# Performance work log

Hardware: AMD Instinct MI355X
Metric: run time of the kernel (lower is better)

Reference implementation:

```python
import jax, jax.numpy as jnp
import numpy as np

D_MODEL = 1024
N_HEADS = 16
D_HEAD = D_MODEL // N_HEADS
SCALE = D_HEAD ** 0.5
EPS_NORM = 1e-10
EPS_CLAMP = 1e-06


def _sphere(x):
    # project to unit sphere along last dim
    n = jnp.maximum(jnp.linalg.norm(x, axis=-1, keepdims=True), EPS_NORM)
    return x / n


def setup_inputs() -> dict:
    key = jax.random.key(0)
    ks = jax.random.split(key, 9)
    s = 1.0 / np.sqrt(D_MODEL)  # torch Linear default init scale
    inp = {
        "H": jax.random.normal(ks[0], (2, 2048, D_MODEL), dtype=jnp.float32),
        "W_q": jax.random.uniform(ks[1], (D_MODEL, D_MODEL), jnp.float32, -s, s),
        "b_q": jax.random.uniform(ks[2], (D_MODEL,), jnp.float32, -s, s),
        "W_k": jax.random.uniform(ks[3], (D_MODEL, D_MODEL), jnp.float32, -s, s),
        "b_k": jax.random.uniform(ks[4], (D_MODEL,), jnp.float32, -s, s),
        "W_v": jax.random.uniform(ks[5], (D_MODEL, D_MODEL), jnp.float32, -s, s),
        "b_v": jax.random.uniform(ks[6], (D_MODEL,), jnp.float32, -s, s),
        "W_o": jax.random.uniform(ks[7], (D_MODEL, D_MODEL), jnp.float32, -s, s),
        "b_o": jax.random.uniform(ks[8], (D_MODEL,), jnp.float32, -s, s),
    }
    return inp


def reference(H, W_q, b_q, W_k, b_k, W_v, b_v, W_o, b_o):
    B, S, _ = H.shape
    # torch Linear: y = x @ W.T + b
    def proj(W, b):
        y = jnp.einsum('bsd,ed->bse', H, W) + b
        return _sphere(y.reshape(B, S, N_HEADS, D_HEAD).transpose(0, 2, 1, 3))  # [B,H,S,Dh]
    Q = proj(W_q, b_q)
    K = proj(W_k, b_k)
    V = proj(W_v, b_v)
    cos = jnp.einsum('bhqd,bhkd->bhqk', Q, K)
    cos = jnp.clip(cos, -1.0 + EPS_CLAMP, 1.0 - EPS_CLAMP)
    scores = -jnp.arccos(cos) / SCALE
    attn = jax.nn.softmax(scores, axis=-1)
    out = jnp.einsum('bhqk,bhkd->bhqd', attn, V)
    out = out.transpose(0, 2, 1, 3).reshape(B, S, D_MODEL)
    return jnp.einsum('bsd,ed->bse', out, W_o) + b_o
```

## Files before the change

### kernel.cpp

```cpp
#include <hip/hip_runtime.h>
#include <hip/hip_bf16.h>

typedef __bf16 bf16_t;
typedef __bf16 bf16x8 __attribute__((ext_vector_type(8)));
typedef __bf16 bf16x4 __attribute__((ext_vector_type(4)));
typedef float f32x2 __attribute__((ext_vector_type(2)));
typedef float f32x4 __attribute__((ext_vector_type(4)));
typedef float f32x16 __attribute__((ext_vector_type(16)));

#define NB 2
#define SEQ 2048
#define DMODEL 1024
#define NHEAD 16
#define DHEAD 64

#define PSWAP(x, y) asm("v_permlane32_swap_b32 %0, %1" : "+v"(x), "+v"(y))
#define CVTPK(d, a, b) asm("v_cvt_pk_bf16_f32 %0, %1, %2" : "=v"(d) : "v"(a), "v"(b))
#define WAITVM(n) asm volatile("s_waitcnt vmcnt(" #n ")" ::: "memory")

__device__ inline void gload_lds16(const void* g, void* lds) {
  __builtin_amdgcn_global_load_lds((const __attribute__((address_space(1))) void*)g,
                                   (__attribute__((address_space(3))) void*)lds,
                                   16, 0, 0);
}

__global__ __launch_bounds__(256) void cvt_all_kernel(
    const float* __restrict__ H,  const float* __restrict__ Wq, const float* __restrict__ Wk,
    const float* __restrict__ Wv, const float* __restrict__ Wo,
    bf16_t* __restrict__ Hb, bf16_t* __restrict__ Wqb, bf16_t* __restrict__ Wkb,
    bf16_t* __restrict__ Wvb, bf16_t* __restrict__ Wob)
{
  const int b = blockIdx.x;
  const float* src; bf16_t* dst; int idx;
  if (b < 4096) { src = H; dst = Hb; idx = b; }
  else {
    const int r = b - 4096; const int s = r >> 10; idx = r & 1023;
    src = (s == 0) ? Wq : (s == 1) ? Wk : (s == 2) ? Wv : Wo;
    dst = (s == 0) ? Wqb : (s == 1) ? Wkb : (s == 2) ? Wvb : Wob;
  }
  const int i = idx * 256 + threadIdx.x;
  float4 v = ((const float4*)src)[i];
  bf16x4 o;
  o[0] = (bf16_t)v.x; o[1] = (bf16_t)v.y; o[2] = (bf16_t)v.z; o[3] = (bf16_t)v.w;
  ((bf16x4*)dst)[i] = o;
}

template<int MODE>
__global__ __launch_bounds__(256, 3) void gemm_bt_kernel(
    const bf16_t* __restrict__ A,
    const bf16_t* __restrict__ W0, const bf16_t* __restrict__ W1, const bf16_t* __restrict__ W2,
    const float* __restrict__ bias0, const float* __restrict__ bias1, const float* __restrict__ bias2,
    void* out0, void* out1, void* out2)
{
  __shared__ char gsm[49152];
  const int tid = threadIdx.x;
  const int lane = tid & 63;
  const int w = tid >> 6;
  const int mt = blockIdx.y, nt = blockIdx.x, z = blockIdx.z;
  const bf16_t* Wp = (z == 0) ? W0 : ((z == 1) ? W1 : W2);
  const float* bp  = (z == 0) ? bias0 : ((z == 1) ? bias1 : bias2);

  const int wr = w & 1, wc = w >> 1;
  const int fr = lane & 15, fq = lane >> 4;

  const int r_in = lane >> 3;
  const int cswz = ((lane & 7) ^ (r_in & 7)) << 4;

  f32x4 acc[2][4] = {};

  const char* Ab = (const char*)(A + (size_t)mt * 64 * DMODEL);
  const char* Bb = (const char*)(Wp + (size_t)nt * 128 * DMODEL);

  const unsigned aA0 = (unsigned)__builtin_amdgcn_readfirstlane(w * 2048);
  const unsigned bB0 = (unsigned)__builtin_amdgcn_readfirstlane(16384 + w * 4096);

  #define GSTAGE(t, buf)                                                                   \
    do {                                                                                   \
      const size_t k0b_ = (size_t)(t) * 128;                                               \
      _Pragma("unroll")                                                                    \
      for (int i = 0; i < 2; ++i) {                                                        \
        const size_t rowA_ = (size_t)(w * 16 + i * 8 + r_in);                              \
        gload_lds16(Ab + rowA_ * (DMODEL * 2) + k0b_ + cswz,                               \
                    gsm + aA0 + (buf) * 8192 + i * 1024);                                  \
      }                                                                                    \
      _Pragma("unroll")                                                                    \
      for (int i = 0; i < 4; ++i) {                                                        \
        const size_t rowB_ = (size_t)(w * 32 + i * 8 + r_in);                              \
        gload_lds16(Bb + rowB_ * (DMODEL * 2) + k0b_ + cswz,                               \
                    gsm + bB0 + (buf) * 16384 + i * 1024);                                 \
      }                                                                                    \
    } while (0)

  #define GCOMPUTE(buf)                                                                    \
    do {                                                                                   \
      const char* As_ = gsm + (buf) * 8192;                                                \
      const char* Bs_ = gsm + 16384 + (buf) * 16384;                                       \
      bf16x8 a_[2][2], b_[4][2];                                                           \
      _Pragma("unroll")                                                                    \
      for (int m = 0; m < 2; ++m)                                                          \
        _Pragma("unroll")                                                                  \
        for (int ks = 0; ks < 2; ++ks)                                                     \
          a_[m][ks] = *(const bf16x8*)(As_ + (wr * 32 + m * 16 + fr) * 128 +               \
                                       ((ks * 64 + fq * 16) ^ ((fr & 7) << 4)));           \
      _Pragma("unroll")                                                                    \
      for (int n = 0; n < 4; ++n)                                                          \
        _Pragma("unroll")                                                                  \
        for (int ks = 0; ks < 2; ++ks)                                                     \
          b_[n][ks] = *(const bf16x8*)(Bs_ + (wc * 64 + n * 16 + fr) * 128 +               \
                                       ((ks * 64 + fq * 16) ^ ((fr & 7) << 4)));           \
      __builtin_amdgcn_s_setprio(1);                                                       \
      _Pragma("unroll")                                                                    \
      for (int m = 0; m < 2; ++m)                                                          \
        _Pragma("unroll")                                                                  \
        for (int n = 0; n < 4; ++n)                                                        \
          _Pragma("unroll")                                                                \
          for (int ks = 0; ks < 2; ++ks)                                                   \
            acc[m][n] = __builtin_amdgcn_mfma_f32_16x16x32_bf16(a_[m][ks], b_[n][ks],      \
                                                                acc[m][n], 0, 0, 0);       \
      __builtin_amdgcn_s_setprio(0);                                                       \
    } while (0)

  GSTAGE(0, 0);
  GSTAGE(1, 1);
  for (int t2 = 0; t2 < 7; ++t2) {
    WAITVM(6);
    __builtin_amdgcn_s_barrier();
    GCOMPUTE(0);
    __builtin_amdgcn_s_barrier();
    GSTAGE(2 * t2 + 2, 0);
    WAITVM(6);
    __builtin_amdgcn_s_barrier();
    GCOMPUTE(1);
    __builtin_amdgcn_s_barrier();
    GSTAGE(2 * t2 + 3, 1);
  }
  WAITVM(6);
  __builtin_amdgcn_s_barrier();
  GCOMPUTE(0);
  WAITVM(0);
  __builtin_amdgcn_s_barrier();
  GCOMPUTE(1);
  #undef GCOMPUTE
  #undef GSTAGE

  float bv[4];
  const int cb = nt * 128 + wc * 64;
  #pragma unroll
  for (int n = 0; n < 4; ++n) bv[n] = bp[cb + n * 16 + fr];

  if constexpr (MODE == 0) {
    float* outp = (float*)out0;
    #pragma unroll
    for (int m = 0; m < 2; ++m) {
      #pragma unroll
      for (int j = 0; j < 4; ++j) {
        const int row = mt * 64 + wr * 32 + m * 16 + fq * 4 + j;
        float* orow = outp + (size_t)row * DMODEL + cb;
        #pragma unroll
        for (int n = 0; n < 4; ++n)
          orow[n * 16 + fr] = acc[m][n][j] + bv[n];
      }
    }
  } else {
    const int h = nt * 2 + wc;
    if (z < 2) {
      #pragma unroll
      for (int m = 0; m < 2; ++m) {
        #pragma unroll
        for (int j = 0; j < 4; ++j) {
          float v0 = acc[m][0][j] + bv[0];
          float v1 = acc[m][1][j] + bv[1];
          float v2 = acc[m][2][j] + bv[2];
          float v3 = acc[m][3][j] + bv[3];
          float ss = v0 * v0 + v1 * v1 + v2 * v2 + v3 * v3;
          ss += __shfl_xor(ss, 1);
          ss += __shfl_xor(ss, 2);
          ss += __shfl_xor(ss, 4);
          ss += __shfl_xor(ss, 8);
          const float inv = 1.0f / fmaxf(sqrtf(ss), 1e-10f);
          const int row = mt * 64 + wr * 32 + m * 16 + fq * 4 + j;
          const int bb = row >> 11, sr = row & (SEQ - 1);
          bf16_t* op = ((z == 0) ? (bf16_t*)out0 : (bf16_t*)out1)
                       + (((size_t)(bb * NHEAD + h)) * SEQ + sr) * DHEAD;
          op[0 * 16 + fr] = (bf16_t)(v0 * inv);
          op[1 * 16 + fr] = (bf16_t)(v1 * inv);
          op[2 * 16 + fr] = (bf16_t)(v2 * inv);
          op[3 * 16 + fr] = (bf16_t)(v3 * inv);
        }
      }
    } else {
      __syncthreads();
      bf16_t* vt = (bf16_t*)gsm;
      #pragma unroll
      for (int m = 0; m < 2; ++m) {
        #pragma unroll
        for (int j = 0; j < 4; ++j) {
          float v0 = acc[m][0][j] + bv[0];
          float v1 = acc[m][1][j] + bv[1];
          float v2 = acc[m][2][j] + bv[2];
          float v3 = acc[m][3][j] + bv[3];
          float ss = v0 * v0 + v1 * v1 + v2 * v2 + v3 * v3;
          ss += __shfl_xor(ss, 1);
          ss += __shfl_xor(ss, 2);
          ss += __shfl_xor(ss, 4);
          ss += __shfl_xor(ss, 8);
          const float inv = 1.0f / fmaxf(sqrtf(ss), 1e-10f);
          const int r64 = wr * 32 + m * 16 + fq * 4 + j;
          vt[r64 * 128 + wc * 64 + 0 * 16 + fr] = (bf16_t)(v0 * inv);
          vt[r64 * 128 + wc * 64 + 1 * 16 + fr] = (bf16_t)(v1 * inv);
          vt[r64 * 128 + wc * 64 + 2 * 16 + fr] = (bf16_t)(v2 * inv);
          vt[r64 * 128 + wc * 64 + 3 * 16 + fr] = (bf16_t)(v3 * inv);
        }
      }
      __syncthreads();
      const int bb16 = (mt >> 5) * 16;
      const int srbase = (mt & 31) * 64;
      #pragma unroll
      for (int p = 0; p < 4; ++p) {
        const int id = p * 256 + tid;
        const int c = id >> 3;
        const int sc = (id & 7) * 8;
        bf16x8 vv;
        #pragma unroll
        for (int i = 0; i < 8; ++i)
          vv[i] = vt[(sc + i) * 128 + c];
        const int hh = nt * 2 + (c >> 6);
        const int dh = c & 63;
        bf16_t* gp = (bf16_t*)out2 + (((size_t)(bb16 + hh)) * 64 + dh) * (size_t)SEQ + srbase + sc;
        *(bf16x8*)gp = vv;
      }
    }
  }
}

__device__ inline f32x16 sp16(float x) {
  f32x16 v;
  #pragma unroll
  for (int i = 0; i < 16; ++i) v[i] = x;
  return v;
}

__device__ inline void score_pack(const f32x16& accp, float& l_acc, bf16x8& pf0, bf16x8& pf1) {
  const f32x16 c2 = accp * accp;
  f32x16 a = __builtin_elementwise_fma(c2, sp16(0.00379774f), sp16(0.00558036f));
  a = __builtin_elementwise_fma(c2, a, sp16(0.00937500f));
  a = __builtin_elementwise_fma(c2, a, sp16(0.02083333f));
  a = __builtin_elementwise_fma(c2, a, sp16(0.12500000f));
  const f32x16 s = a * accp;
  f32x16 e = __builtin_elementwise_fma(s, sp16(0.16666667f), sp16(0.5f));
  e = __builtin_elementwise_fma(s, e, sp16(1.0f));
  e = __builtin_elementwise_fma(s, e, sp16(1.0f));
  const float t0 = (e[0] + e[1]) + (e[2] + e[3]);
  const float t1 = (e[4] + e[5]) + (e[6] + e[7]);
  const float t2 = (e[8] + e[9]) + (e[10] + e[11]);
  const float t3 = (e[12] + e[13]) + (e[14] + e[15]);
  l_acc += (t0 + t1) + (t2 + t3);
  unsigned dwA0, dwA1, dwA2, dwA3, dwB0, dwB1, dwB2, dwB3;
  CVTPK(dwA0, e[0], e[1]);   CVTPK(dwB0, e[2], e[3]);
  CVTPK(dwA1, e[4], e[5]);   CVTPK(dwB1, e[6], e[7]);
  CVTPK(dwA2, e[8], e[9]);   CVTPK(dwB2, e[10], e[11]);
  CVTPK(dwA3, e[12], e[13]); CVTPK(dwB3, e[14], e[15]);
  PSWAP(dwA0, dwA1);  PSWAP(dwB0, dwB1);
  PSWAP(dwA2, dwA3);  PSWAP(dwB2, dwB3);
  typedef unsigned u32x4_ __attribute__((ext_vector_type(4)));
  u32x4_ t0_ = { dwA0, dwB0, dwA1, dwB1 };
  u32x4_ t1_ = { dwA2, dwB2, dwA3, dwB3 };
  pf0 = __builtin_bit_cast(bf16x8, t0_);
  pf1 = __builtin_bit_cast(bf16x8, t1_);
}

__global__ __launch_bounds__(512, 2) void mfma_attn_kernel(
    const bf16_t* __restrict__ Qb, const bf16_t* __restrict__ Kb,
    const bf16_t* __restrict__ Vt, bf16_t* __restrict__ Oat)
{
  __shared__ char smem[65536];

  const int tid = threadIdx.x;
  const int lane = tid & 63;
  const int w = tid >> 6;
  const int qw = w & 3, kh = w >> 2;
  const int l31 = lane & 31, l5 = lane >> 5;

  const int p = blockIdx.x;
  const int xcd = p & 7;
  const int j = p >> 3;
  const int bh = xcd * 4 + (j >> 4);
  const int qt = j & 15;
  const int q0 = qt * 128 + qw * 32;
  const int NT = 16;

  const bf16_t* Qp = Qb + ((size_t)bh * SEQ + q0 + l31) * DHEAD + l5 * 8;
  bf16x8 b_q[4];
  #pragma unroll
  for (int m = 0; m < 4; ++m)
    b_q[m] = *(const bf16x8*)(Qp + m * 16);

  const char* KbaseH = (const char*)(Kb + (size_t)bh * SEQ * DHEAD) + (size_t)kh * 1024 * DHEAD * 2;
  const char* VbaseH = (const char*)(Vt + (size_t)bh * DHEAD * SEQ) + (size_t)kh * 1024 * 2;

  const int chA = 2 * qw, chB = 2 * qw + 1;
  int koffA, koffB, voffA, voffB;
  {
    const int rA = chA * 4 + (lane >> 4), rB = chB * 4 + (lane >> 4);
    const int c = (lane & 15) * 16;
    const int cpA = c ^ ((rA & 15) << 4), cpB = c ^ ((rB & 15) << 4);
    koffA = (rA + ((cpA >> 7) << 5)) * 128 + (cpA & 127);
    koffB = (rB + ((cpB >> 7) << 5)) * 128 + (cpB & 127);
    voffA = (rA + ((cpA >> 7) << 5)) * (SEQ * 2) + (cpA & 127);
    voffB = (rB + ((cpB >> 7) << 5)) * (SEQ * 2) + (cpB & 127);
  }
  const unsigned stKA = (unsigned)__builtin_amdgcn_readfirstlane(kh * 32768 + chA * 1024);
  const unsigned stKB = (unsigned)__builtin_amdgcn_readfirstlane(kh * 32768 + chB * 1024);
  const unsigned rb0  = (unsigned)__builtin_amdgcn_readfirstlane(kh * 32768);

  const int swz = (l31 & 15) << 4;
  const unsigned kRow = l31 * 256;

  f32x16 acc_o0 = {}, acc_o1 = {};
  float l_acc = 0.0f;

  #define STAGE(t, buf)                                                                    \
    do {                                                                                   \
      const char* Kt_ = KbaseH + (size_t)(t) * 8192;                                       \
      const char* Vc_ = VbaseH + (size_t)(t) * 128;                                        \
      gload_lds16(Kt_ + koffA, smem + stKA + (buf) * 16384);                               \
      gload_lds16(Kt_ + koffB, smem + stKB + (buf) * 16384);                               \
      gload_lds16(Vc_ + voffA, smem + stKA + (buf) * 16384 + 8192);                        \
      gload_lds16(Vc_ + voffB, smem + stKB + (buf) * 16384 + 8192);                        \
    } while (0)

  #define TILE(buf)                                                                        \
    do {                                                                                   \
      const char* kb_ = smem + rb0 + (buf) * 16384 + kRow;                                 \
      const char* vb_ = smem + rb0 + (buf) * 16384 + 8192 + kRow;                          \
      f32x16 accp0 = {}, accp1 = {};                                                       \
      _Pragma("unroll")                                                                    \
      for (int m = 0; m < 4; ++m) {                                                        \
        bf16x8 akA = *(const bf16x8*)(kb_ + ((m * 32 + l5 * 16) ^ swz));                   \
        bf16x8 akB = *(const bf16x8*)(kb_ + ((128 + m * 32 + l5 * 16) ^ swz));             \
        accp0 = __builtin_amdgcn_mfma_f32_32x32x16_bf16(akA, b_q[m], accp0, 0, 0, 0);      \
        accp1 = __builtin_amdgcn_mfma_f32_32x32x16_bf16(akB, b_q[m], accp1, 0, 0, 0);      \
      }                                                                                    \
      {                                                                                    \
        bf16x8 pf0, pf1;                                                                   \
        score_pack(accp0, l_acc, pf0, pf1);                                                \
        bf16x8 av00 = *(const bf16x8*)(vb_ + ((  0 + l5 * 16) ^ swz));                     \
        bf16x8 av01 = *(const bf16x8*)(vb_ + (( 32 + l5 * 16) ^ swz));                     \
        bf16x8 av10 = *(const bf16x8*)(vb_ + ((128 +  0 + l5 * 16) ^ swz));                \
        bf16x8 av11 = *(const bf16x8*)(vb_ + ((128 + 32 + l5 * 16) ^ swz));                \
        acc_o0 = __builtin_amdgcn_mfma_f32_32x32x16_bf16(av00, pf0, acc_o0, 0, 0, 0);      \
        acc_o1 = __builtin_amdgcn_mfma_f32_32x32x16_bf16(av10, pf0, acc_o1, 0, 0, 0);      \
        acc_o0 = __builtin_amdgcn_mfma_f32_32x32x16_bf16(av01, pf1, acc_o0, 0, 0, 0);      \
        acc_o1 = __builtin_amdgcn_mfma_f32_32x32x16_bf16(av11, pf1, acc_o1, 0, 0, 0);      \
      }                                                                                    \
      {                                                                                    \
        bf16x8 pf0, pf1;                                                                   \
        score_pack(accp1, l_acc, pf0, pf1);                                                \
        bf16x8 av00 = *(const bf16x8*)(vb_ + (( 64 +  0 + l5 * 16) ^ swz));                \
        bf16x8 av01 = *(const bf16x8*)(vb_ + (( 64 + 32 + l5 * 16) ^ swz));                \
        bf16x8 av10 = *(const bf16x8*)(vb_ + ((128 + 64 +  0 + l5 * 16) ^ swz));           \
        bf16x8 av11 = *(const bf16x8*)(vb_ + ((128 + 64 + 32 + l5 * 16) ^ swz));           \
        acc_o0 = __builtin_amdgcn_mfma_f32_32x32x16_bf16(av00, pf0, acc_o0, 0, 0, 0);      \
        acc_o1 = __builtin_amdgcn_mfma_f32_32x32x16_bf16(av10, pf0, acc_o1, 0, 0, 0);      \
        acc_o0 = __builtin_amdgcn_mfma_f32_32x32x16_bf16(av01, pf1, acc_o0, 0, 0, 0);      \
        acc_o1 = __builtin_amdgcn_mfma_f32_32x32x16_bf16(av11, pf1, acc_o1, 0, 0, 0);      \
      }                                                                                    \
    } while (0)

  STAGE(0, 0);
  STAGE(1, 1);

  for (int t2 = 0; t2 < NT / 2 - 1; ++t2) {
    WAITVM(4);
    __builtin_amdgcn_s_barrier();
    TILE(0);
    __builtin_amdgcn_s_barrier();
    STAGE(2 * t2 + 2, 0);
    WAITVM(4);
    __builtin_amdgcn_s_barrier();
    TILE(1);
    __builtin_amdgcn_s_barrier();
    STAGE(2 * t2 + 3, 1);
  }
  WAITVM(4);
  __builtin_amdgcn_s_barrier();
  TILE(0);
  WAITVM(0);
  __builtin_amdgcn_s_barrier();
  TILE(1);
  #undef TILE
  #undef STAGE

  l_acc += __shfl_xor(l_acc, 32);

  __syncthreads();
  float* cO = (float*)smem;
  float* cL = (float*)(smem + 32768);
  if (kh == 1) {
    #pragma unroll
    for (int r = 0; r < 16; ++r) {
      cO[(qw * 32 + r) * 64 + lane] = acc_o0[r];
      cO[(qw * 32 + 16 + r) * 64 + lane] = acc_o1[r];
    }
    cL[qw * 64 + lane] = l_acc;
  }
  __syncthreads();
  if (kh == 0) {
    #pragma unroll
    for (int r = 0; r < 16; ++r) {
      acc_o0[r] += cO[(qw * 32 + r) * 64 + lane];
      acc_o1[r] += cO[(qw * 32 + 16 + r) * 64 + lane];
    }
    l_acc += cL[qw * 64 + lane];
    const float invl = __builtin_amdgcn_rcpf(l_acc);
    const int bb = bh >> 4, h = bh & 15;
    bf16_t* op = Oat + ((size_t)bb * SEQ + q0 + l31) * DMODEL + h * DHEAD;
    #pragma unroll
    for (int blk = 0; blk < 2; ++blk) {
      const f32x16& ao = blk ? acc_o1 : acc_o0;
      #pragma unroll
      for (int g = 0; g < 4; ++g) {
        bf16x4 ov;
        ov[0] = (bf16_t)(ao[4 * g + 0] * invl);
        ov[1] = (bf16_t)(ao[4 * g + 1] * invl);
        ov[2] = (bf16_t)(ao[4 * g + 2] * invl);
        ov[3] = (bf16_t)(ao[4 * g + 3] * invl);
        *(bf16x4*)(op + blk * 32 + 8 * g + 4 * l5) = ov;
      }
    }
  }
}

extern "C" void kernel_launch(void* const* d_in, const int* in_sizes, int n_in,
                              void* d_out, int out_size, void* d_ws, size_t ws_size,
                              hipStream_t stream)
{
  const float* H  = (const float*)d_in[0];
  const float* Wq = (const float*)d_in[1];
  const float* bq = (const float*)d_in[2];
  const float* Wk = (const float*)d_in[3];
  const float* bk = (const float*)d_in[4];
  const float* Wv = (const float*)d_in[5];
  const float* bv = (const float*)d_in[6];
  const float* Wo = (const float*)d_in[7];
  const float* bo = (const float*)d_in[8];
  float* out = (float*)d_out;

  char* ws = (char*)d_ws;
  bf16_t* Hb  = (bf16_t*)(ws);
  bf16_t* Wqb = (bf16_t*)(ws + (8u << 20));
  bf16_t* Wkb = (bf16_t*)(ws + (10u << 20));
  bf16_t* Wvb = (bf16_t*)(ws + (12u << 20));
  bf16_t* Wob = (bf16_t*)(ws + (14u << 20));
  bf16_t* Qbf = (bf16_t*)(ws + (16u << 20));
  bf16_t* Kbf = (bf16_t*)(ws + (24u << 20));
  bf16_t* Vtb = (bf16_t*)(ws + (32u << 20));
  bf16_t* Oat = (bf16_t*)(ws + (40u << 20));

  cvt_all_kernel<<<8192, 256, 0, stream>>>(H, Wq, Wk, Wv, Wo, Hb, Wqb, Wkb, Wvb, Wob);

  gemm_bt_kernel<1><<<dim3(8, 64, 3), 256, 0, stream>>>(
      Hb, Wqb, Wkb, Wvb, bq, bk, bv, Qbf, Kbf, Vtb);

  mfma_attn_kernel<<<512, 512, 0, stream>>>(Qbf, Kbf, Vtb, Oat);

  gemm_bt_kernel<0><<<dim3(8, 64, 1), 256, 0, stream>>>(
      Oat, Wob, Wob, Wob, bo, bo, bo, out, out, out);
}
```

Measured before the change: 123.0 us.

## Split attention waves into producer score and consumer PV groups via LDS

Replaces the split-KV scheme, where two wave groups each handled half the keys and merged results at the end, with warp specialization. Four producer waves compute QK^T scores and the arccos/softmax packing and write P tiles to LDS. Four consumer waves, running one tile behind at raised priority, read P and V and do the PV MFMAs. This aims to overlap the transcendental score math with the PV matrix work and to drop the final cross-group accumulator reduction. In exchange it adds LDS traffic for P, more barriers per tile, and a 32-step serialized loop.

```diff
diff --git a/kernel.cpp b/kernel.cpp
--- a/kernel.cpp
+++ b/kernel.cpp
@@ -4,7 +4,6 @@
 typedef __bf16 bf16_t;
 typedef __bf16 bf16x8 __attribute__((ext_vector_type(8)));
 typedef __bf16 bf16x4 __attribute__((ext_vector_type(4)));
-typedef float f32x2 __attribute__((ext_vector_type(2)));
 typedef float f32x4 __attribute__((ext_vector_type(4)));
 typedef float f32x16 __attribute__((ext_vector_type(16)));
 
@@ -17,6 +16,7 @@
 #define PSWAP(x, y) asm("v_permlane32_swap_b32 %0, %1" : "+v"(x), "+v"(y))
 #define CVTPK(d, a, b) asm("v_cvt_pk_bf16_f32 %0, %1, %2" : "=v"(d) : "v"(a), "v"(b))
 #define WAITVM(n) asm volatile("s_waitcnt vmcnt(" #n ")" ::: "memory")
+#define WAITLGKM0 asm volatile("s_waitcnt lgkmcnt(0)" ::: "memory")
 
 __device__ inline void gload_lds16(const void* g, void* lds) {
   __builtin_amdgcn_global_load_lds((const __attribute__((address_space(1))) void*)g,
@@ -278,27 +278,30 @@
   const int tid = threadIdx.x;
   const int lane = tid & 63;
   const int w = tid >> 6;
-  const int qw = w & 3, kh = w >> 2;
+  const bool prod = (w < 4);
+  const int g = w & 3;
   const int l31 = lane & 31, l5 = lane >> 5;
+  const int NT = 32;
 
   const int p = blockIdx.x;
   const int xcd = p & 7;
   const int j = p >> 3;
   const int bh = xcd * 4 + (j >> 4);
   const int qt = j & 15;
-  const int q0 = qt * 128 + qw * 32;
-  const int NT = 16;
-
-  const bf16_t* Qp = Qb + ((size_t)bh * SEQ + q0 + l31) * DHEAD + l5 * 8;
+  const int q0 = qt * 128 + g * 32;
+
   bf16x8 b_q[4];
-  #pragma unroll
-  for (int m = 0; m < 4; ++m)
-    b_q[m] = *(const bf16x8*)(Qp + m * 16);
-
-  const char* KbaseH = (const char*)(Kb + (size_t)bh * SEQ * DHEAD) + (size_t)kh * 1024 * DHEAD * 2;
-  const char* VbaseH = (const char*)(Vt + (size_t)bh * DHEAD * SEQ) + (size_t)kh * 1024 * 2;
-
-  const int chA = 2 * qw, chB = 2 * qw + 1;
+  if (prod) {
+    const bf16_t* Qp = Qb + ((size_t)bh * SEQ + q0 + l31) * DHEAD + l5 * 8;
+    #pragma unroll
+    for (int m = 0; m < 4; ++m)
+      b_q[m] = *(const bf16x8*)(Qp + m * 16);
+  }
+
+  const char* Kbase = (const char*)(Kb + (size_t)bh * SEQ * DHEAD);
+  const char* Vbase = (const char*)(Vt + (size_t)bh * DHEAD * SEQ);
+
+  const int chA = 2 * g, chB = 2 * g + 1;
   int koffA, koffB, voffA, voffB;
   {
     const int rA = chA * 4 + (lane >> 4), rB = chB * 4 + (lane >> 4);
@@ -309,9 +312,9 @@
     voffA = (rA + ((cpA >> 7) << 5)) * (SEQ * 2) + (cpA & 127);
     voffB = (rB + ((cpB >> 7) << 5)) * (SEQ * 2) + (cpB & 127);
   }
-  const unsigned stKA = (unsigned)__builtin_amdgcn_readfirstlane(kh * 32768 + chA * 1024);
-  const unsigned stKB = (unsigned)__builtin_amdgcn_readfirstlane(kh * 32768 + chB * 1024);
-  const unsigned rb0  = (unsigned)__builtin_amdgcn_readfirstlane(kh * 32768);
+  const unsigned chAo = (unsigned)__builtin_amdgcn_readfirstlane(chA * 1024);
+  const unsigned chBo = (unsigned)__builtin_amdgcn_readfirstlane(chB * 1024);
+  const unsigned pgo  = (unsigned)__builtin_amdgcn_readfirstlane(32768 + g * 4096);
 
   const int swz = (l31 & 15) << 4;
   const unsigned kRow = l31 * 256;
@@ -319,20 +322,23 @@
   f32x16 acc_o0 = {}, acc_o1 = {};
   float l_acc = 0.0f;
 
-  #define STAGE(t, buf)                                                                    \
-    do {                                                                                   \
-      const char* Kt_ = KbaseH + (size_t)(t) * 8192;                                       \
-      const char* Vc_ = VbaseH + (size_t)(t) * 128;                                        \
-      gload_lds16(Kt_ + koffA, smem + stKA + (buf) * 16384);                               \
-      gload_lds16(Kt_ + koffB, smem + stKB + (buf) * 16384);                               \
-      gload_lds16(Vc_ + voffA, smem + stKA + (buf) * 16384 + 8192);                        \
-      gload_lds16(Vc_ + voffB, smem + stKB + (buf) * 16384 + 8192);                        \
-    } while (0)
-
-  #define TILE(buf)                                                                        \
-    do {                                                                                   \
-      const char* kb_ = smem + rb0 + (buf) * 16384 + kRow;                                 \
-      const char* vb_ = smem + rb0 + (buf) * 16384 + 8192 + kRow;                          \
+  #define STAGE_K(t, buf)                                                                  \
+    do {                                                                                   \
+      const char* Kt_ = Kbase + (size_t)(t) * 8192;                                        \
+      gload_lds16(Kt_ + koffA, smem + (buf) * 8192 + chAo);                                \
+      gload_lds16(Kt_ + koffB, smem + (buf) * 8192 + chBo);                                \
+    } while (0)
+
+  #define STAGE_V(t, buf)                                                                  \
+    do {                                                                                   \
+      const char* Vc_ = Vbase + (size_t)(t) * 128;                                         \
+      gload_lds16(Vc_ + voffA, smem + 16384 + (buf) * 8192 + chAo);                        \
+      gload_lds16(Vc_ + voffB, smem + 16384 + (buf) * 8192 + chBo);                        \
+    } while (0)
+
+  #define PROD_TILE(buf)                                                                   \
+    do {                                                                                   \
+      const char* kb_ = smem + (buf) * 8192 + kRow;                                        \
       f32x16 accp0 = {}, accp1 = {};                                                       \
       _Pragma("unroll")                                                                    \
       for (int m = 0; m < 4; ++m) {                                                        \
@@ -341,94 +347,94 @@
         accp0 = __builtin_amdgcn_mfma_f32_32x32x16_bf16(akA, b_q[m], accp0, 0, 0, 0);      \
         accp1 = __builtin_amdgcn_mfma_f32_32x32x16_bf16(akB, b_q[m], accp1, 0, 0, 0);      \
       }                                                                                    \
+      char* Pw = smem + pgo + (buf) * 16384 + lane * 16;                                   \
       {                                                                                    \
         bf16x8 pf0, pf1;                                                                   \
         score_pack(accp0, l_acc, pf0, pf1);                                                \
-        bf16x8 av00 = *(const bf16x8*)(vb_ + ((  0 + l5 * 16) ^ swz));                     \
-        bf16x8 av01 = *(const bf16x8*)(vb_ + (( 32 + l5 * 16) ^ swz));                     \
-        bf16x8 av10 = *(const bf16x8*)(vb_ + ((128 +  0 + l5 * 16) ^ swz));                \
-        bf16x8 av11 = *(const bf16x8*)(vb_ + ((128 + 32 + l5 * 16) ^ swz));                \
-        acc_o0 = __builtin_amdgcn_mfma_f32_32x32x16_bf16(av00, pf0, acc_o0, 0, 0, 0);      \
-        acc_o1 = __builtin_amdgcn_mfma_f32_32x32x16_bf16(av10, pf0, acc_o1, 0, 0, 0);      \
-        acc_o0 = __builtin_amdgcn_mfma_f32_32x32x16_bf16(av01, pf1, acc_o0, 0, 0, 0);      \
-        acc_o1 = __builtin_amdgcn_mfma_f32_32x32x16_bf16(av11, pf1, acc_o1, 0, 0, 0);      \
+        *(bf16x8*)(Pw + 0)    = pf0;                                                       \
+        *(bf16x8*)(Pw + 1024) = pf1;                                                       \
       }                                                                                    \
       {                                                                                    \
         bf16x8 pf0, pf1;                                                                   \
         score_pack(accp1, l_acc, pf0, pf1);                                                \
-        bf16x8 av00 = *(const bf16x8*)(vb_ + (( 64 +  0 + l5 * 16) ^ swz));                \
-        bf16x8 av01 = *(const bf16x8*)(vb_ + (( 64 + 32 + l5 * 16) ^ swz));                \
-        bf16x8 av10 = *(const bf16x8*)(vb_ + ((128 + 64 +  0 + l5 * 16) ^ swz));           \
-        bf16x8 av11 = *(const bf16x8*)(vb_ + ((128 + 64 + 32 + l5 * 16) ^ swz));           \
-        acc_o0 = __builtin_amdgcn_mfma_f32_32x32x16_bf16(av00, pf0, acc_o0, 0, 0, 0);      \
-        acc_o1 = __builtin_amdgcn_mfma_f32_32x32x16_bf16(av10, pf0, acc_o1, 0, 0, 0);      \
-        acc_o0 = __builtin_amdgcn_mfma_f32_32x32x16_bf16(av01, pf1, acc_o0, 0, 0, 0);      \
-        acc_o1 = __builtin_amdgcn_mfma_f32_32x32x16_bf16(av11, pf1, acc_o1, 0, 0, 0);      \
+        *(bf16x8*)(Pw + 2048) = pf0;                                                       \
+        *(bf16x8*)(Pw + 3072) = pf1;                                                       \
       }                                                                                    \
-    } while (0)
-
-  STAGE(0, 0);
-  STAGE(1, 1);
-
-  for (int t2 = 0; t2 < NT / 2 - 1; ++t2) {
-    WAITVM(4);
-    __builtin_amdgcn_s_barrier();
-    TILE(0);
-    __builtin_amdgcn_s_barrier();
-    STAGE(2 * t2 + 2, 0);
-    WAITVM(4);
-    __builtin_amdgcn_s_barrier();
-    TILE(1);
-    __builtin_amdgcn_s_barrier();
-    STAGE(2 * t2 + 3, 1);
-  }
-  WAITVM(4);
+      WAITLGKM0;                                                                           \
+    } while (0)
+
+  #define CONS_TILE(buf)                                                                   \
+    do {                                                                                   \
+      const char* Pr = smem + pgo + (buf) * 16384 + lane * 16;                             \
+      bf16x8 pf00 = *(const bf16x8*)(Pr + 0);                                              \
+      bf16x8 pf01 = *(const bf16x8*)(Pr + 1024);                                           \
+      bf16x8 pf10 = *(const bf16x8*)(Pr + 2048);                                           \
+      bf16x8 pf11 = *(const bf16x8*)(Pr + 3072);                                           \
+      const char* vb_ = smem + 16384 + (buf) * 8192 + kRow;                                \
+      bf16x8 av00 = *(const bf16x8*)(vb_ + ((  0 + l5 * 16) ^ swz));                       \
+      bf16x8 av01 = *(const bf16x8*)(vb_ + (( 32 + l5 * 16) ^ swz));                       \
+      bf16x8 av10 = *(const bf16x8*)(vb_ + ((128 +  0 + l5 * 16) ^ swz));                  \
+      bf16x8 av11 = *(const bf16x8*)(vb_ + ((128 + 32 + l5 * 16) ^ swz));                  \
+      bf16x8 bv00 = *(const bf16x8*)(vb_ + (( 64 +  0 + l5 * 16) ^ swz));                  \
+      bf16x8 bv01 = *(const bf16x8*)(vb_ + (( 64 + 32 + l5 * 16) ^ swz));                  \
+      bf16x8 bv10 = *(const bf16x8*)(vb_ + ((128 + 64 +  0 + l5 * 16) ^ swz));             \
+      bf16x8 bv11 = *(const bf16x8*)(vb_ + ((128 + 64 + 32 + l5 * 16) ^ swz));             \
+      __builtin_amdgcn_s_setprio(1);                                                       \
+      acc_o0 = __builtin_amdgcn_mfma_f32_32x32x16_bf16(av00, pf00, acc_o0, 0, 0, 0);       \
+      acc_o1 = __builtin_amdgcn_mfma_f32_32x32x16_bf16(av10, pf00, acc_o1, 0, 0, 0);       \
+      acc_o0 = __builtin_amdgcn_mfma_f32_32x32x16_bf16(av01, pf01, acc_o0, 0, 0, 0);       \
+      acc_o1 = __builtin_amdgcn_mfma_f32_32x32x16_bf16(av11, pf01, acc_o1, 0, 0, 0);       \
+      acc_o0 = __builtin_amdgcn_mfma_f32_32x32x16_bf16(bv00, pf10, acc_o0, 0, 0, 0);       \
+      acc_o1 = __builtin_amdgcn_mfma_f32_32x32x16_bf16(bv10, pf10, acc_o1, 0, 0, 0);       \
+      acc_o0 = __builtin_amdgcn_mfma_f32_32x32x16_bf16(bv01, pf11, acc_o0, 0, 0, 0);       \
+      acc_o1 = __builtin_amdgcn_mfma_f32_32x32x16_bf16(bv11, pf11, acc_o1, 0, 0, 0);       \
+      __builtin_amdgcn_s_setprio(0);                                                       \
+    } while (0)
+
+  if (prod) { STAGE_K(0, 0); STAGE_K(1, 1); }
+  else      { STAGE_V(0, 0); }
+
+  for (int t = 0; t < NT; ++t) {
+    if (t < NT - 2) { WAITVM(2); } else { WAITVM(0); }
+    __builtin_amdgcn_s_barrier();
+    if (prod) PROD_TILE(t & 1);
+    else if (t > 0) CONS_TILE((t - 1) & 1);
+    __builtin_amdgcn_s_barrier();
+    if (prod) { if (t < NT - 2) STAGE_K(t + 2, t & 1); }
+    else      { if (t < NT - 1) STAGE_V(t + 1, (t + 1) & 1); }
+  }
+  if (prod) {
+    l_acc += __shfl_xor(l_acc, 32);
+    if (lane < 32) ((float*)(smem + 32768))[g * 32 + l31] = l_acc;
+    WAITLGKM0;
+  } else {
+    CONS_TILE((NT - 1) & 1);
+  }
   __builtin_amdgcn_s_barrier();
-  TILE(0);
-  WAITVM(0);
-  __builtin_amdgcn_s_barrier();
-  TILE(1);
-  #undef TILE
-  #undef STAGE
-
-  l_acc += __shfl_xor(l_acc, 32);
-
-  __syncthreads();
-  float* cO = (float*)smem;
-  float* cL = (float*)(smem + 32768);
-  if (kh == 1) {
-    #pragma unroll
-    for (int r = 0; r < 16; ++r) {
-      cO[(qw * 32 + r) * 64 + lane] = acc_o0[r];
-      cO[(qw * 32 + 16 + r) * 64 + lane] = acc_o1[r];
-    }
-    cL[qw * 64 + lane] = l_acc;
-  }
-  __syncthreads();
-  if (kh == 0) {
-    #pragma unroll
-    for (int r = 0; r < 16; ++r) {
-      acc_o0[r] += cO[(qw * 32 + r) * 64 + lane];
-      acc_o1[r] += cO[(qw * 32 + 16 + r) * 64 + lane];
-    }
-    l_acc += cL[qw * 64 + lane];
-    const float invl = __builtin_amdgcn_rcpf(l_acc);
+
+  if (!prod) {
+    const float lq = ((const float*)(smem + 32768))[g * 32 + l31];
+    const float invl = __builtin_amdgcn_rcpf(lq);
     const int bb = bh >> 4, h = bh & 15;
     bf16_t* op = Oat + ((size_t)bb * SEQ + q0 + l31) * DMODEL + h * DHEAD;
     #pragma unroll
     for (int blk = 0; blk < 2; ++blk) {
       const f32x16& ao = blk ? acc_o1 : acc_o0;
       #pragma unroll
-      for (int g = 0; g < 4; ++g) {
+      for (int gg = 0; gg < 4; ++gg) {
         bf16x4 ov;
-        ov[0] = (bf16_t)(ao[4 * g + 0] * invl);
-        ov[1] = (bf16_t)(ao[4 * g + 1] * invl);
-        ov[2] = (bf16_t)(ao[4 * g + 2] * invl);
-        ov[3] = (bf16_t)(ao[4 * g + 3] * invl);
-        *(bf16x4*)(op + blk * 32 + 8 * g + 4 * l5) = ov;
+        ov[0] = (bf16_t)(ao[4 * gg + 0] * invl);
+        ov[1] = (bf16_t)(ao[4 * gg + 1] * invl);
+        ov[2] = (bf16_t)(ao[4 * gg + 2] * invl);
+        ov[3] = (bf16_t)(ao[4 * gg + 3] * invl);
+        *(bf16x4*)(op + blk * 32 + 8 * gg + 4 * l5) = ov;
       }
     }
   }
+  #undef CONS_TILE
+  #undef PROD_TILE
+  #undef STAGE_V
+  #undef STAGE_K
 }
 
 extern "C" void kernel_launch(void* const* d_in, const int* in_sizes, int n_in,
```

New measurement: 136.7 us. 11.2% more time.
